# Optimization experiments

Measured on AMD Instinct MI355X. Metric: run time of the kernel, lower is better.

The kernel has to match this reference:

```python
import math
import jax, jax.numpy as jnp
import numpy as np

# ---- static config (mirrors init_kwargs) ----
NLAT_I, NLON_I = 240, 480      # input equiangular grid (incl. both poles)
NLAT_O, NLON_O = 361, 720      # output equiangular grid (incl. both poles)
CI, CO = 32, 32
NR, NPHI = 3, 3                # kernel_shape
K = (NR - 1) * NPHI + 1        # anisotropic piecewise-linear DISCO basis size = 7
LMAX = 120
CUTOFF = (NR + 0.25) * math.pi / LMAX     # _compute_cutoff_radius
DLAT_O = math.pi / (NLAT_O - 1)
WOFF = int(math.ceil(CUTOFF / DLAT_O))    # half lat-window (=10); geodesic dist >= |dtheta| so window is exact
WLAT = 2 * WOFF + 1
TWO_PI = 2.0 * math.pi


def _bilinear_upsample(x):
    # ResampleS2(mode='bilinear'): x [B,C,NLAT_I,NLON_I] -> [B,C,NLAT_O,NLON_O]
    # equiangular colatitudes theta_j = pi*j/(nlat-1); periodic longitude.
    pos_t = jnp.linspace(0.0, math.pi, NLAT_O) / (math.pi / (NLAT_I - 1))
    i0 = jnp.clip(jnp.floor(pos_t).astype(jnp.int32), 0, NLAT_I - 1)
    i1 = jnp.minimum(i0 + 1, NLAT_I - 1)
    wt = (pos_t - i0).astype(x.dtype)
    xl = (1.0 - wt)[:, None] * x[:, :, i0, :] + wt[:, None] * x[:, :, i1, :]
    pos_p = (jnp.arange(NLON_O) * (TWO_PI / NLON_O)) / (TWO_PI / NLON_I)
    j0f = jnp.floor(pos_p)
    j0 = j0f.astype(jnp.int32) % NLON_I
    j1 = (j0 + 1) % NLON_I
    wp = (pos_p - j0f).astype(x.dtype)
    return (1.0 - wp) * xl[..., j0] + wp * xl[..., j1]


def _build_psi():
    # DISCO filter tensor psi[k, t_out, dlat, dlon] with quadrature merged in,
    # exploiting longitude translation invariance (computed at lon_out = 0).
    theta = jnp.linspace(0.0, math.pi, NLAT_O)
    t_idx = jnp.arange(NLAT_O)
    d_idx = jnp.arange(WLAT) - WOFF
    lat_in = t_idx[:, None] + d_idx[None, :]             # [T,W]
    valid = (lat_in >= 0) & (lat_in < NLAT_O)
    lat_in_c = jnp.clip(lat_in, 0, NLAT_O - 1)
    alpha = -theta[:, None, None]                         # [T,1,1]
    gamma = theta[lat_in_c][:, :, None]                   # [T,W,1]
    beta = (TWO_PI / NLON_O) * jnp.arange(NLON_O)[None, None, :]
    # rotate input point into frame where the output point is at the north pole
    z = jnp.cos(alpha) * jnp.cos(gamma) - jnp.cos(beta) * jnp.sin(alpha) * jnp.sin(gamma)
    xx = jnp.cos(alpha) * jnp.cos(beta) * jnp.sin(gamma) + jnp.sin(alpha) * jnp.cos(gamma)
    yy = jnp.sin(beta) * jnp.sin(gamma)
    r = jnp.arccos(jnp.clip(z, -1.0, 1.0))                # geodesic distance [T,W,P]
    phi = jnp.arctan2(yy, xx) % TWO_PI                    # local azimuth
    dr = CUTOFF / NR
    dph = TWO_PI / NPHI
    vals = [jnp.maximum(0.0, 1.0 - r / dr)]               # isotropic center hat
    for k in range(1, K):
        ir = (k - 1) // NPHI + 1
        ip = (k - 1) % NPHI
        rad = jnp.maximum(0.0, 1.0 - jnp.abs(r - ir * dr) / dr)
        dd = jnp.abs(phi - ip * dph)
        dd = jnp.minimum(dd, TWO_PI - dd)
        az = jnp.maximum(0.0, 1.0 - dd / dph)
        vals.append(rad * az)
    psi = jnp.stack(vals, 0)                              # [K,T,W,P]
    psi = psi * (r <= CUTOFF) * valid[None, :, :, None]
    # merge quadrature weights of the input grid (sin(theta) dtheta dphi)
    q = jnp.sin(theta) * (math.pi / (NLAT_O - 1)) * (TWO_PI / NLON_O)
    psi = psi * q[lat_in_c][None, :, :, None]
    # nodal L1 normalization per basis function and output node
    scale = jnp.sum(psi, axis=(2, 3), keepdims=True)
    psi = psi / jnp.maximum(scale, 1e-8)
    return psi.astype(jnp.float32), lat_in_c


def _disco_conv(xu, weight, psi, lat_in_c):
    # xu [B,Ci,T,P]; weight [Co,Ci,K]; psi [K,T,W,P]
    h = jnp.einsum('oik,bitp->boktp', weight, xu)         # fold channel mixing first
    Hh = jnp.fft.rfft(h, axis=-1)                         # [B,Co,K,T,F]
    Ph = jnp.conj(jnp.fft.rfft(psi, axis=-1))             # [K,T,W,F]
    yh = jnp.zeros(Hh.shape[:2] + (NLAT_O, Hh.shape[-1]), dtype=Hh.dtype)
    for d in range(WLAT):                                 # small fixed halo loop
        Hd = Hh[:, :, :, lat_in_c[:, d], :]               # [B,Co,K,T,F]
        yh = yh + jnp.einsum('boktf,ktf->botf', Hd, Ph[:, :, d, :])
    return jnp.fft.irfft(yh, n=NLON_O, axis=-1)           # circular correlation over lon


def setup_inputs() -> dict:
    key = jax.random.key(0)
    k1, k2 = jax.random.split(key)
    x = jax.random.normal(k1, (1, CI, NLAT_I, NLON_I), dtype=jnp.float32)
    weight = jax.random.normal(k2, (CO, CI, K), dtype=jnp.float32) * 0.05
    return {'x': x, 'weight': weight}


def reference(x, weight):
    psi, lat_in_c = _build_psi()
    xu = _bilinear_upsample(x.astype(jnp.float32))        # forced fp32 region
    y = _disco_conv(xu, weight.astype(jnp.float32), psi, lat_in_c)
    return y.astype(x.dtype)
```

## Files before the change

kernel.cpp:

```cpp
#include <hip/hip_runtime.h>
#include <hip/hip_bf16.h>
#include <math.h>

#define NLAT_I 240
#define NLON_I 480
#define NLAT_O 361
#define NLON_O 720
#define CI_N 32
#define CO_N 32
#define K_N 7
#define WOFF 10
#define WLAT 21

#define PI_F 3.14159265358979323846f
#define TWOPI_F 6.28318530717958647692f
#define DLAT_V (PI_F / 360.0f)
#define DPHI_V (TWOPI_F / 720.0f)
#define CUTOFF_V (3.25f * PI_F / 120.0f)
#define DR_V (CUTOFF_V / 3.0f)
#define IDR_V (1.0f / DR_V)
#define DPH_V (TWOPI_F / 3.0f)
#define IDPH_V (1.0f / DPH_V)
#define QF_V (DLAT_V * DPHI_V)

#define PAD_T 64
#define CT 128
#define NBLK 256
#define NC45 45
#define NE 7581

typedef __attribute__((ext_vector_type(8))) short short8v;
typedef __attribute__((ext_vector_type(4))) short short4v;
typedef __attribute__((ext_vector_type(16))) float f32x16;

__device__ __forceinline__ unsigned short f2bf(float f) {
  __hip_bfloat16 h = __float2bfloat16(f);
  union { __hip_bfloat16 b; unsigned short s; } u; u.b = h; return u.s;
}

typedef __attribute__((address_space(1))) const unsigned int ga_u32_t;
typedef __attribute__((address_space(3))) unsigned int ls_u32_t;
__device__ __forceinline__ void dma16(const unsigned short* g, unsigned short* l) {
  __builtin_amdgcn_global_load_lds((ga_u32_t*)(const void*)g,
                                   (ls_u32_t*)(void*)l, 16, 0, 0);
}

__device__ __forceinline__ void psi_eval(float ct, float st, float cg, float sg,
                                         float q, float bang, float v[7]) {
  float sb, cb;
  sincosf(bang, &sb, &cb);
  float dx = sg * cb - st;
  float dy = sg * sb;
  float dz = cg - ct;
  float c2 = dx * dx + dy * dy + dz * dz;
  float r = 2.0f * asinf(fminf(1.0f, 0.5f * sqrtf(c2)));
  if (r <= CUTOFF_V) {
    float xx = ct * cb * sg - st * cg;
    float yy = sb * sg;
    float phi = atan2f(yy, xx);
    if (phi < 0.0f) phi += TWOPI_F;
    v[0] = fmaxf(0.0f, 1.0f - r * IDR_V) * q;
#pragma unroll
    for (int k = 1; k < 7; ++k) {
      const float irdr = (float)(1 + (k - 1) / 3) * DR_V;
      const float ipph = (float)((k - 1) % 3) * DPH_V;
      float rad = fmaxf(0.0f, 1.0f - fabsf(r - irdr) * IDR_V);
      float dd = fabsf(phi - ipph);
      dd = fminf(dd, TWOPI_F - dd);
      float az = fmaxf(0.0f, 1.0f - dd * IDPH_V);
      v[k] = rad * az * q;
    }
  } else {
#pragma unroll
    for (int k = 0; k < 7; ++k) v[k] = 0.0f;
  }
}

__device__ __forceinline__ int windowB(int t, int d) {
  int tp = t + d - WOFF;
  if (tp < 0 || tp > NLAT_O - 1) return -1;
  float th = (float)t * DLAT_V, ga = (float)tp * DLAT_V;
  float st = sinf(th), ct = cosf(th), sg = sinf(ga), cg = cosf(ga);
  float den = st * sg;
  float num = cosf(CUTOFF_V) - ct * cg;
  if (den < 1e-9f) return (fabsf(th - ga) <= CUTOFF_V) ? 360 : -1;
  if (num >= den) return -1;
  if (num <= -den) return 360;
  int B = (int)ceilf(acosf(num / den) * (1.0f / DPHI_V)) + 1;
  return B > 360 ? 360 : B;
}

__device__ __forceinline__ int nsupOf(int B) { return (B >= 360) ? 720 : 2 * B + 1; }
__device__ __forceinline__ int widthOf(int B) {
  return (B < 0) ? 0 : ((nsupOf(B) + 129) & ~1);
}

__global__ void prep_kernel(const float* __restrict__ w, unsigned short* __restrict__ w2,
                            int* __restrict__ offsF, int* __restrict__ offsT,
                            int* __restrict__ wtab, float* __restrict__ sums,
                            int* __restrict__ counter, int* __restrict__ gB,
                            int* __restrict__ gUc) {
  const int tid = threadIdx.x;
  __shared__ int temp[256];
  if (tid < 8) counter[tid] = 0;
  for (int idx = tid; idx < 361 * 7; idx += 256) sums[idx] = 0.0f;
  for (int idx = tid; idx < 14 * 32 * 16; idx += 256) {
    int kk = idx & 15; int o = (idx >> 4) & 31; int c16 = idx >> 9;
    int il = 4 * (kk >> 3) + (kk & 3) + 8 * ((kk >> 2) & 1);
    int i = (c16 & 1) * 16 + il; int k = c16 >> 1;
    w2[idx] = f2bf(w[(o * 32 + i) * 7 + k]);
  }
  for (int e = tid; e < NE; e += 256) {
    int t = e / 21, d = e % 21;
    int B = windowB(t, d);
    gB[e] = B;
    offsF[e] = (B >= 0) ? nsupOf(B) * 7 : 0;
    offsT[e] = 14 * widthOf(B);
  }
  __syncthreads();
  for (int t = tid; t < 361; t += 256) {
    int run = 0;
    for (int d = 0; d < WLAT; ++d) {
      gUc[t * 22 + d] = run;
      int B = gB[t * 21 + d];
      int np = (B >= 0) ? ((31 + B) >> 4) + ((B + 15) >> 4) + 1 : 0;
      run += np;
    }
    gUc[t * 22 + 21] = run;
    wtab[t] = run;
  }
  __syncthreads();
#pragma unroll 1
  for (int pass = 0; pass < 2; ++pass) {
    int* a = pass ? offsT : offsF;
    int s = tid * 30, e = s + 30; if (e > NE) e = NE; if (s > NE) s = NE;
    int sum = 0;
    for (int i = s; i < e; ++i) sum += a[i];
    temp[tid] = sum;
    __syncthreads();
    if (tid == 0) {
      int run = 0;
      for (int i = 0; i < 256; ++i) { int v = temp[i]; temp[i] = run; run += v; }
      a[NE] = run;
    }
    __syncthreads();
    int run = temp[tid];
    for (int i = s; i < e; ++i) { int v = a[i]; a[i] = run; run += v; }
    __syncthreads();
  }
}

__global__ void upsample_kernel(const float* __restrict__ x,
                                unsigned short* __restrict__ XT) {
  int idx = blockIdx.x * 256 + threadIdx.x;
  if (idx >= NLAT_O * NC45 * 512) return;
  int kk = idx & 15;
  int i = (idx >> 4) & 31;
  int c = (idx >> 9) % NC45;
  int t = idx / (NC45 * 512);
  int p = c * 16 + kk;

  double post = (double)t * (239.0 / 360.0);
  int i0 = (int)floor(post);
  if (i0 < 0) i0 = 0;
  if (i0 > NLAT_I - 1) i0 = NLAT_I - 1;
  int i1 = i0 + 1; if (i1 > NLAT_I - 1) i1 = NLAT_I - 1;
  float wt = (float)(post - (double)i0);

  double posp = (double)p * (2.0 / 3.0);
  double j0f = floor(posp);
  int j0 = ((int)j0f) % NLON_I;
  int j1 = (j0 + 1) % NLON_I;
  float wp = (float)(posp - j0f);

  const float* xi = x + (size_t)i * (NLAT_I * NLON_I);
  float a = xi[i0 * NLON_I + j0];
  float b = xi[i0 * NLON_I + j1];
  float cc = xi[i1 * NLON_I + j0];
  float d = xi[i1 * NLON_I + j1];
  float l0 = (1.0f - wt) * a + wt * cc;
  float l1 = (1.0f - wt) * b + wt * d;
  XT[idx] = f2bf((1.0f - wp) * l0 + wp * l1);
}

__global__ void psi_raw_kernel(const int* __restrict__ offsF,
                               float* __restrict__ PSIF,
                               float* __restrict__ sums) {
  int t = blockIdx.x, d = blockIdx.y;
  int B = windowB(t, d);
  if (B < 0) return;
  int nsup = nsupOf(B);
  int bLo = (B >= 360) ? -360 : -B;
  int offF = offsF[t * 21 + d];
  int tp = t + d - WOFF;
  float th = (float)t * DLAT_V, ga = (float)tp * DLAT_V;
  float st, ct, sg, cg;
  sincosf(th, &st, &ct);
  sincosf(ga, &sg, &cg);
  float q = sg * QF_V;
  float acc[7];
#pragma unroll
  for (int k = 0; k < 7; ++k) acc[k] = 0.0f;
  for (int ix = threadIdx.x; ix < nsup; ix += 256) {
    float v[7];
    psi_eval(ct, st, cg, sg, q, (float)(bLo + ix) * DPHI_V, v);
#pragma unroll
    for (int k = 0; k < 7; ++k) { PSIF[offF + k * nsup + ix] = v[k]; acc[k] += v[k]; }
  }
#pragma unroll
  for (int k = 0; k < 7; ++k) {
    float a = acc[k];
    for (int off = 32; off > 0; off >>= 1) a += __shfl_down(a, off, 64);
    acc[k] = a;
  }
  __shared__ float red[4][7];
  int wid = threadIdx.x >> 6;
  if ((threadIdx.x & 63) == 0) {
#pragma unroll
    for (int k = 0; k < 7; ++k) red[wid][k] = acc[k];
  }
  __syncthreads();
  if (threadIdx.x == 0) {
#pragma unroll
    for (int k = 0; k < 7; ++k)
      atomicAdd(&sums[t * 7 + k], red[0][k] + red[1][k] + red[2][k] + red[3][k]);
  }
}

__global__ void psi_toep_kernel(const int* __restrict__ offsF,
                                const int* __restrict__ offsT,
                                const float* __restrict__ PSIF,
                                const float* __restrict__ sums,
                                unsigned short* __restrict__ PSIT) {
  int t = blockIdx.x, d = blockIdx.y;
  int B = windowB(t, d);
  if (B < 0) return;
  int nsup = nsupOf(B);
  int width = widthOf(B);
  int offF = offsF[t * 21 + d];
  int offT = offsT[t * 21 + d];
  float rc[7];
#pragma unroll
  for (int k = 0; k < 7; ++k) rc[k] = 1.0f / fmaxf(sums[t * 7 + k], 1e-8f);
  for (int ix = threadIdx.x; ix <= width; ix += 256) {
    int isup = ix - PAD_T;
    unsigned short vv[7];
    if (isup >= 0 && isup < nsup) {
#pragma unroll
      for (int k = 0; k < 7; ++k)
        vv[k] = f2bf(PSIF[offF + k * nsup + isup] * rc[k]);
    } else {
#pragma unroll
      for (int k = 0; k < 7; ++k) vv[k] = 0;
    }
    if (ix < width) {
#pragma unroll
      for (int k = 0; k < 7; ++k) PSIT[offT + (2 * k) * width + ix] = vv[k];
    }
    if (ix >= 1) {
#pragma unroll
      for (int k = 0; k < 7; ++k) PSIT[offT + (2 * k + 1) * width + ix - 1] = vv[k];
    }
  }
}


#define VMW8 asm volatile("s_waitcnt vmcnt(8)" ::: "memory");
#define BARR  __builtin_amdgcn_s_barrier();

#define GETMETA(IX) \
    int mx_, my_; \
    if ((IX) & 64) { mx_ = __builtin_amdgcn_readlane(mxL1, (IX) & 63); \
                     my_ = __builtin_amdgcn_readlane(myL1, (IX) & 63); } \
    else           { mx_ = __builtin_amdgcn_readlane(mxL0, (IX) & 63); \
                     my_ = __builtin_amdgcn_readlane(myL0, (IX) & 63); }

#define STAGEU(IDX) {                                                       \
    int ix_ = (IDX); if (ix_ > nUm1) ix_ = nUm1;                            \
    GETMETA(ix_)                                                            \
    int wdt_ = my_ & 4095;                                                  \
    int dd_ = (my_ >> 12) & 31;                                             \
    int cc_ = ((my_ >> 17) & 63) - 32;                                      \
    int sl_ = ix_ & 7;                                                      \
    int jb_ = mx_ + lconst;                                                 \
    const unsigned short* bs_ = PSIT + jb_ + ((jb_ & 1) ? (wdt_ - 1) : 0);  \
    unsigned short* bd_ = Bring + sl_ * 3584;                               \
    int ks_ = 2 * wdt_;                                                     \
    dma16(bs_ + r0B * ks_, bd_ + (r0B << 9));                               \
    dma16(bs_ + r1B * ks_, bd_ + (r1B << 9));                               \
    int v45_ = pw16 + cc_;                                                  \
    if (v45_ < 0) v45_ += NC45;                                             \
    if (v45_ >= NC45) v45_ -= NC45;                                         \
    int v45b_ = v45_ + 2; if (v45b_ >= NC45) v45b_ -= NC45;                 \
    int tpd_ = t + dd_ - WOFF;                                              \
    unsigned short* ad_ = Aring + (((wv << 3) + sl_) << 10);                \
    dma16(XT + (((size_t)(tpd_ * NC45 + v45_)) << 9) + laneA, ad_);         \
    dma16(XT + (((size_t)(tpd_ * NC45 + v45b_)) << 9) + laneA, ad_ + 512); }

#define READF(S, IDX) {                                                     \
    int sl_ = (IDX) & 7;                                                    \
    const unsigned short* bb_ = Bring + sl_ * 3584 + (lane << 3);           \
    B##S##0 = *(const short8v*)(bb_);                                       \
    B##S##1 = *(const short8v*)(bb_ + 512);                                 \
    B##S##2 = *(const short8v*)(bb_ + 1024);                                \
    B##S##3 = *(const short8v*)(bb_ + 1536);                                \
    B##S##4 = *(const short8v*)(bb_ + 2048);                                \
    B##S##5 = *(const short8v*)(bb_ + 2560);                                \
    B##S##6 = *(const short8v*)(bb_ + 3072);                                \
    const unsigned short* aa_ = Aring + (((wv << 3) + sl_) << 10) + (lane << 3); \
    A##S##a = *(const short8v*)(aa_);                                       \
    A##S##b = *(const short8v*)(aa_ + 512); }

#define MFMA14(S) {                                                         \
    accA0 = __builtin_amdgcn_mfma_f32_32x32x16_bf16(A##S##a, B##S##0, accA0, 0, 0, 0); \
    accB0 = __builtin_amdgcn_mfma_f32_32x32x16_bf16(A##S##b, B##S##0, accB0, 0, 0, 0); \
    accA1 = __builtin_amdgcn_mfma_f32_32x32x16_bf16(A##S##a, B##S##1, accA1, 0, 0, 0); \
    accB1 = __builtin_amdgcn_mfma_f32_32x32x16_bf16(A##S##b, B##S##1, accB1, 0, 0, 0); \
    accA2 = __builtin_amdgcn_mfma_f32_32x32x16_bf16(A##S##a, B##S##2, accA2, 0, 0, 0); \
    accB2 = __builtin_amdgcn_mfma_f32_32x32x16_bf16(A##S##b, B##S##2, accB2, 0, 0, 0); \
    accA3 = __builtin_amdgcn_mfma_f32_32x32x16_bf16(A##S##a, B##S##3, accA3, 0, 0, 0); \
    accB3 = __builtin_amdgcn_mfma_f32_32x32x16_bf16(A##S##b, B##S##3, accB3, 0, 0, 0); \
    accA4 = __builtin_amdgcn_mfma_f32_32x32x16_bf16(A##S##a, B##S##4, accA4, 0, 0, 0); \
    accB4 = __builtin_amdgcn_mfma_f32_32x32x16_bf16(A##S##b, B##S##4, accB4, 0, 0, 0); \
    accA5 = __builtin_amdgcn_mfma_f32_32x32x16_bf16(A##S##a, B##S##5, accA5, 0, 0, 0); \
    accB5 = __builtin_amdgcn_mfma_f32_32x32x16_bf16(A##S##b, B##S##5, accB5, 0, 0, 0); \
    accA6 = __builtin_amdgcn_mfma_f32_32x32x16_bf16(A##S##a, B##S##6, accA6, 0, 0, 0); \
    accB6 = __builtin_amdgcn_mfma_f32_32x32x16_bf16(A##S##b, B##S##6, accB6, 0, 0, 0); }

#define DUMP2(ACC, KK, HB) {                                              \
    short8v q_;                                                           \
    q_[0]=(short)f2bf(ACC[8*(HB)+0]); q_[1]=(short)f2bf(ACC[8*(HB)+1]);   \
    q_[2]=(short)f2bf(ACC[8*(HB)+2]); q_[3]=(short)f2bf(ACC[8*(HB)+3]);   \
    q_[4]=(short)f2bf(ACC[8*(HB)+4]); q_[5]=(short)f2bf(ACC[8*(HB)+5]);   \
    q_[6]=(short)f2bf(ACC[8*(HB)+6]); q_[7]=(short)f2bf(ACC[8*(HB)+7]);   \
    *(short8v*)(b2 + ((KK) << 9) + b0_) = q_; }

#define GEMM2PT(AC0, AC1, AC2, AC3, AC4, AC5, AC6, PTILE) {               \
    f32x16 Dy;                                                            \
    _Pragma("unroll") for (int z = 0; z < 16; ++z) Dy[z] = 0.0f;          \
    DUMP2(AC0, 0, 0) DUMP2(AC1, 1, 0) DUMP2(AC2, 2, 0) DUMP2(AC3, 3, 0)  \
    DUMP2(AC4, 4, 0) DUMP2(AC5, 5, 0) DUMP2(AC6, 6, 0)                    \
    _Pragma("unroll") for (int k2 = 0; k2 < 7; ++k2) {                    \
      short8v A2 = *(const short8v*)(w2g + (((2 * k2 + 0) * 32 + nn) << 4) + g8); \
      short8v B2f = *(const short8v*)(b2 + (k2 << 9) + (nn << 4) + g8);   \
      Dy = __builtin_amdgcn_mfma_f32_32x32x16_bf16(A2, B2f, Dy, 0, 0, 0); \
    }                                                                     \
    DUMP2(AC0, 0, 1) DUMP2(AC1, 1, 1) DUMP2(AC2, 2, 1) DUMP2(AC3, 3, 1)  \
    DUMP2(AC4, 4, 1) DUMP2(AC5, 5, 1) DUMP2(AC6, 6, 1)                    \
    _Pragma("unroll") for (int k2 = 0; k2 < 7; ++k2) {                    \
      short8v A2 = *(const short8v*)(w2g + (((2 * k2 + 1) * 32 + nn) << 4) + g8); \
      short8v B2f = *(const short8v*)(b2 + (k2 << 9) + (nn << 4) + g8);   \
      Dy = __builtin_amdgcn_mfma_f32_32x32x16_bf16(A2, B2f, Dy, 0, 0, 0); \
    }                                                                     \
    const int p_ = (PTILE) * 32 + nn;                                     \
    if (p_ < NLON_O) {                                                    \
      _Pragma("unroll") for (int rr = 0; rr < 16; ++rr) {                 \
        int o = (rr & 3) + 8 * (rr >> 2) + 4 * g;                         \
        atomicAdd(&y[((size_t)o * NLAT_O + t) * NLON_O + p_], Dy[rr]);    \
      }                                                                   \
    } }

__global__ __launch_bounds__(256, 1) void disco_kernel(
    const unsigned short* __restrict__ XT, const unsigned short* __restrict__ PSIT,
    const unsigned short* __restrict__ w2g, const int* __restrict__ offsT,
    const int* __restrict__ wtab, const int* __restrict__ gB,
    const int* __restrict__ gUc, float* __restrict__ y,
    int* __restrict__ counter) {
  const int tid = threadIdx.x;
  __shared__ __align__(16) unsigned short Bring[8 * 3584];
  __shared__ __align__(16) unsigned short Aring[32 * 1024];
  __shared__ __align__(16) unsigned short b2all[4 * 3584];
  __shared__ int Sbuf[362];
  __shared__ int sB[WLAT], sUc[WLAT + 1], sOff[WLAT], sW[WLAT];
  __shared__ int curItem, sSv;

  for (int j = tid; j < 361; j += 256) {
    int t = (j & 1) ? 360 - (j >> 1) : (j >> 1);
    Sbuf[j] = 3 * ((wtab[t] + CT - 1) / CT);
  }
  __syncthreads();
  if (tid == 0) {
    int run = 0;
    for (int j = 0; j < 361; ++j) { int v = Sbuf[j]; Sbuf[j] = run; run += v; }
    Sbuf[361] = run;
    sSv = 0;
  }
  __syncthreads();
  const int NTOT = Sbuf[361];
  const int xcd = blockIdx.x & 7;

  const int lane = tid & 63, wv = tid >> 6, nn = lane & 31, g = lane >> 5;
  const int g8 = g * 8;
  const int laneA = nn * 16 + g8;
  const int lconst = g8 - nn;
  const int r0B = (wv < 3) ? 2 * wv : 6;
  const int r1B = (wv < 3) ? 2 * wv + 1 : 6;

  while (true) {
    if (tid == 0) {
      int mm = NTOT;
      int s2 = sSv;
      while (s2 < 8) {
        int cx = (xcd + s2) & 7;
        int b0 = (NTOT * cx) >> 3;
        int b1 = (NTOT * (cx + 1)) >> 3;
        int off = atomicAdd(&counter[cx], 1);
        if (b0 + off < b1) { mm = b0 + off; break; }
        ++s2;
      }
      sSv = s2;
      curItem = mm;
    }
    __syncthreads();
    const int m = curItem;
    if (m >= NTOT) break;

    int lo = 0, hi = 360;
    while (lo < hi) {
      int mid = (lo + hi + 1) >> 1;
      if (Sbuf[mid] <= m) lo = mid; else hi = mid - 1;
    }
    const int j = lo;
    const int r = m - Sbuf[j];
    const int t = (j & 1) ? 360 - (j >> 1) : (j >> 1);
    const int pgpair = r % 3;
    const int part = r / 3;

    if (tid < WLAT) {
      int B = gB[t * 21 + tid];
      sB[tid] = B;
      sOff[tid] = offsT[t * 21 + tid];
      sW[tid] = widthOf(B);
    }
    if (tid < WLAT + 1) sUc[tid] = gUc[t * 22 + tid];
    __syncthreads();

    const int Wt = sUc[WLAT];
    int g0 = part * CT, g1 = g0 + CT;
    if (g1 > Wt) g1 = Wt;
    const int nU = g1 - g0;
    const int nUm1 = nU - 1;

    const int ptileA = pgpair * 8 + 2 * wv;
    const int pw16 = ptileA * 2;

    int mxL0, myL0, mxL1, myL1;
#pragma unroll
    for (int hfu = 0; hfu < 2; ++hfu) {
      int uu_ = lane + hfu * 64; if (uu_ > nUm1) uu_ = nUm1;
      int ug_ = g0 + uu_;
      int dd = 0;
      while (dd < 20 && sUc[dd + 1] <= ug_) ++dd;
      int Bv = sB[dd];
      int bLo_ = (Bv >= 360) ? -360 : -Bv;
      int cc_ = -((Bv + 15) >> 4) + (ug_ - sUc[dd]);
      int mxv = sOff[dd] + cc_ * 16 - bLo_ + PAD_T;
      int myv = sW[dd] | (dd << 12) | ((cc_ + 32) << 17);
      if (hfu == 0) { mxL0 = mxv; myL0 = myv; } else { mxL1 = mxv; myL1 = myv; }
    }

    f32x16 accA0, accA1, accA2, accA3, accA4, accA5, accA6;
    f32x16 accB0, accB1, accB2, accB3, accB4, accB5, accB6;
#pragma unroll
    for (int z = 0; z < 16; ++z) {
      accA0[z]=0; accA1[z]=0; accA2[z]=0; accA3[z]=0; accA4[z]=0; accA5[z]=0; accA6[z]=0;
      accB0[z]=0; accB1[z]=0; accB2[z]=0; accB3[z]=0; accB4[z]=0; accB5[z]=0; accB6[z]=0;
    }

    short8v AXa, AXb, BX0, BX1, BX2, BX3, BX4, BX5, BX6;
    short8v AYa, AYb, BY0, BY1, BY2, BY3, BY4, BY5, BY6;

    STAGEU(0) STAGEU(1) STAGEU(2) STAGEU(3)
    VMW8 BARR
    READF(X, 0)

    int u = 0;
    while (true) {
      STAGEU(u + 4) STAGEU(u + 5)
      VMW8 BARR
      int nx = u + 1; bool h1 = (nx < nU); if (!h1) nx = u;
      READF(Y, nx)
      MFMA14(X)
      if (!h1) break;
      int nx2 = u + 2; bool h2 = (nx2 < nU); if (!h2) nx2 = nx;
      READF(X, nx2)
      MFMA14(Y)
      if (!h2) break;
      u += 2;
    }

    unsigned short* b2 = b2all + wv * 3584;
    const int b0_ = nn * 16 + g8;
    GEMM2PT(accA0, accA1, accA2, accA3, accA4, accA5, accA6, ptileA)
    GEMM2PT(accB0, accB1, accB2, accB3, accB4, accB5, accB6, ptileA + 1)
  }
}

extern "C" void kernel_launch(void* const* d_in, const int* in_sizes, int n_in,
                              void* d_out, int out_size, void* d_ws, size_t ws_size,
                              hipStream_t stream) {
  (void)in_sizes; (void)n_in; (void)out_size; (void)ws_size;
  const float* x = (const float*)d_in[0];
  const float* w = (const float*)d_in[1];
  float* y = (float*)d_out;

  unsigned short* XT = (unsigned short*)d_ws;
  float* PSIF = (float*)(XT + (size_t)NLAT_O * NC45 * 512);
  unsigned short* PSIT = (unsigned short*)(PSIF + 6000000);
  unsigned short* w2 = PSIT + 26000000;
  float* sums = (float*)(w2 + 7168);
  int* offsF = (int*)(sums + NLAT_O * K_N);
  int* offsT = offsF + NE + 1;
  int* wtab = offsT + NE + 1;
  int* counter = wtab + 361;
  int* gB = counter + 8;
  int* gUc = gB + NE;

  hipMemsetAsync(y, 0, (size_t)CO_N * NLAT_O * NLON_O * sizeof(float), stream);

  prep_kernel<<<1, 256, 0, stream>>>(w, w2, offsF, offsT, wtab, sums, counter, gB, gUc);
  int n_up = NLAT_O * NC45 * 512;
  upsample_kernel<<<(n_up + 255) / 256, 256, 0, stream>>>(x, XT);
  psi_raw_kernel<<<dim3(NLAT_O, WLAT), 256, 0, stream>>>(offsF, PSIF, sums);
  psi_toep_kernel<<<dim3(NLAT_O, WLAT), 256, 0, stream>>>(offsF, offsT, PSIF, sums, PSIT);
  disco_kernel<<<NBLK, 256, 0, stream>>>(XT, PSIT, w2, offsT, wtab, gB, gUc, y, counter);
}
```

Baseline: 478.0 us.

## Widen per-wave register tile to three longitude tiles, reusing psi fragments

Each wave now accumulates three 32-wide longitude tiles instead of two. Each psi B fragment read from LDS therefore feeds three MFMAs rather than two, and work items per latitude are regrouped from thirds into halves. To make room for the wider A ring, the separate epilogue scratch buffer is dropped and the second-stage GEMM now stages through the wave's own A-ring slots. This adds 112 accumulator registers and cuts the number of schedulable work items, which may hurt load balance. Async prefetches still in flight when the loop exits could also land on the reused scratch.

```diff
diff --git a/kernel.cpp b/kernel.cpp
--- a/kernel.cpp
+++ b/kernel.cpp
@@ -265,7 +265,7 @@
 }
 
 
-#define VMW8 asm volatile("s_waitcnt vmcnt(8)" ::: "memory");
+#define VMW10 asm volatile("s_waitcnt vmcnt(10)" ::: "memory");
 #define BARR  __builtin_amdgcn_s_barrier();
 
 #define GETMETA(IX) \
@@ -292,10 +292,13 @@
     if (v45_ < 0) v45_ += NC45;                                             \
     if (v45_ >= NC45) v45_ -= NC45;                                         \
     int v45b_ = v45_ + 2; if (v45b_ >= NC45) v45b_ -= NC45;                 \
+    int v45c_ = v45b_ + 2; if (v45c_ >= NC45) v45c_ -= NC45;                \
     int tpd_ = t + dd_ - WOFF;                                              \
-    unsigned short* ad_ = Aring + (((wv << 3) + sl_) << 10);                \
-    dma16(XT + (((size_t)(tpd_ * NC45 + v45_)) << 9) + laneA, ad_);         \
-    dma16(XT + (((size_t)(tpd_ * NC45 + v45b_)) << 9) + laneA, ad_ + 512); }
+    const unsigned short* ab_ = XT + (((size_t)(tpd_ * NC45)) << 9) + laneA; \
+    unsigned short* ad_ = Aring + (((wv << 3) + sl_) * 1536);               \
+    dma16(ab_ + ((size_t)v45_ << 9), ad_);                                  \
+    dma16(ab_ + ((size_t)v45b_ << 9), ad_ + 512);                           \
+    dma16(ab_ + ((size_t)v45c_ << 9), ad_ + 1024); }
 
 #define READF(S, IDX) {                                                     \
     int sl_ = (IDX) & 7;                                                    \
@@ -307,25 +310,33 @@
     B##S##4 = *(const short8v*)(bb_ + 2048);                                \
     B##S##5 = *(const short8v*)(bb_ + 2560);                                \
     B##S##6 = *(const short8v*)(bb_ + 3072);                                \
-    const unsigned short* aa_ = Aring + (((wv << 3) + sl_) << 10) + (lane << 3); \
+    const unsigned short* aa_ = Aring + (((wv << 3) + sl_) * 1536) + (lane << 3); \
     A##S##a = *(const short8v*)(aa_);                                       \
-    A##S##b = *(const short8v*)(aa_ + 512); }
-
-#define MFMA14(S) {                                                         \
+    A##S##b = *(const short8v*)(aa_ + 512);                                 \
+    A##S##c = *(const short8v*)(aa_ + 1024); }
+
+#define MFMA21(S) {                                                         \
     accA0 = __builtin_amdgcn_mfma_f32_32x32x16_bf16(A##S##a, B##S##0, accA0, 0, 0, 0); \
     accB0 = __builtin_amdgcn_mfma_f32_32x32x16_bf16(A##S##b, B##S##0, accB0, 0, 0, 0); \
+    accC0 = __builtin_amdgcn_mfma_f32_32x32x16_bf16(A##S##c, B##S##0, accC0, 0, 0, 0); \
     accA1 = __builtin_amdgcn_mfma_f32_32x32x16_bf16(A##S##a, B##S##1, accA1, 0, 0, 0); \
     accB1 = __builtin_amdgcn_mfma_f32_32x32x16_bf16(A##S##b, B##S##1, accB1, 0, 0, 0); \
+    accC1 = __builtin_amdgcn_mfma_f32_32x32x16_bf16(A##S##c, B##S##1, accC1, 0, 0, 0); \
     accA2 = __builtin_amdgcn_mfma_f32_32x32x16_bf16(A##S##a, B##S##2, accA2, 0, 0, 0); \
     accB2 = __builtin_amdgcn_mfma_f32_32x32x16_bf16(A##S##b, B##S##2, accB2, 0, 0, 0); \
+    accC2 = __builtin_amdgcn_mfma_f32_32x32x16_bf16(A##S##c, B##S##2, accC2, 0, 0, 0); \
     accA3 = __builtin_amdgcn_mfma_f32_32x32x16_bf16(A##S##a, B##S##3, accA3, 0, 0, 0); \
     accB3 = __builtin_amdgcn_mfma_f32_32x32x16_bf16(A##S##b, B##S##3, accB3, 0, 0, 0); \
+    accC3 = __builtin_amdgcn_mfma_f32_32x32x16_bf16(A##S##c, B##S##3, accC3, 0, 0, 0); \
     accA4 = __builtin_amdgcn_mfma_f32_32x32x16_bf16(A##S##a, B##S##4, accA4, 0, 0, 0); \
     accB4 = __builtin_amdgcn_mfma_f32_32x32x16_bf16(A##S##b, B##S##4, accB4, 0, 0, 0); \
+    accC4 = __builtin_amdgcn_mfma_f32_32x32x16_bf16(A##S##c, B##S##4, accC4, 0, 0, 0); \
     accA5 = __builtin_amdgcn_mfma_f32_32x32x16_bf16(A##S##a, B##S##5, accA5, 0, 0, 0); \
     accB5 = __builtin_amdgcn_mfma_f32_32x32x16_bf16(A##S##b, B##S##5, accB5, 0, 0, 0); \
+    accC5 = __builtin_amdgcn_mfma_f32_32x32x16_bf16(A##S##c, B##S##5, accC5, 0, 0, 0); \
     accA6 = __builtin_amdgcn_mfma_f32_32x32x16_bf16(A##S##a, B##S##6, accA6, 0, 0, 0); \
-    accB6 = __builtin_amdgcn_mfma_f32_32x32x16_bf16(A##S##b, B##S##6, accB6, 0, 0, 0); }
+    accB6 = __builtin_amdgcn_mfma_f32_32x32x16_bf16(A##S##b, B##S##6, accB6, 0, 0, 0); \
+    accC6 = __builtin_amdgcn_mfma_f32_32x32x16_bf16(A##S##c, B##S##6, accC6, 0, 0, 0); }
 
 #define DUMP2(ACC, KK, HB) {                                              \
     short8v q_;                                                           \
@@ -368,15 +379,14 @@
     int* __restrict__ counter) {
   const int tid = threadIdx.x;
   __shared__ __align__(16) unsigned short Bring[8 * 3584];
-  __shared__ __align__(16) unsigned short Aring[32 * 1024];
-  __shared__ __align__(16) unsigned short b2all[4 * 3584];
+  __shared__ __align__(16) unsigned short Aring[8 * 4 * 1536];
   __shared__ int Sbuf[362];
   __shared__ int sB[WLAT], sUc[WLAT + 1], sOff[WLAT], sW[WLAT];
   __shared__ int curItem, sSv;
 
   for (int j = tid; j < 361; j += 256) {
     int t = (j & 1) ? 360 - (j >> 1) : (j >> 1);
-    Sbuf[j] = 3 * ((wtab[t] + CT - 1) / CT);
+    Sbuf[j] = 2 * ((wtab[t] + CT - 1) / CT);
   }
   __syncthreads();
   if (tid == 0) {
@@ -423,8 +433,8 @@
     const int j = lo;
     const int r = m - Sbuf[j];
     const int t = (j & 1) ? 360 - (j >> 1) : (j >> 1);
-    const int pgpair = r % 3;
-    const int part = r / 3;
+    const int pghalf = r & 1;
+    const int part = r >> 1;
 
     if (tid < WLAT) {
       int B = gB[t * 21 + tid];
@@ -441,7 +451,7 @@
     const int nU = g1 - g0;
     const int nUm1 = nU - 1;
 
-    const int ptileA = pgpair * 8 + 2 * wv;
+    const int ptileA = pghalf * 12 + wv * 3;
     const int pw16 = ptileA * 2;
 
     int mxL0, myL0, mxL1, myL1;
@@ -461,38 +471,41 @@
 
     f32x16 accA0, accA1, accA2, accA3, accA4, accA5, accA6;
     f32x16 accB0, accB1, accB2, accB3, accB4, accB5, accB6;
+    f32x16 accC0, accC1, accC2, accC3, accC4, accC5, accC6;
 #pragma unroll
     for (int z = 0; z < 16; ++z) {
       accA0[z]=0; accA1[z]=0; accA2[z]=0; accA3[z]=0; accA4[z]=0; accA5[z]=0; accA6[z]=0;
       accB0[z]=0; accB1[z]=0; accB2[z]=0; accB3[z]=0; accB4[z]=0; accB5[z]=0; accB6[z]=0;
-    }
-
-    short8v AXa, AXb, BX0, BX1, BX2, BX3, BX4, BX5, BX6;
-    short8v AYa, AYb, BY0, BY1, BY2, BY3, BY4, BY5, BY6;
+      accC0[z]=0; accC1[z]=0; accC2[z]=0; accC3[z]=0; accC4[z]=0; accC5[z]=0; accC6[z]=0;
+    }
+
+    short8v AXa, AXb, AXc, BX0, BX1, BX2, BX3, BX4, BX5, BX6;
+    short8v AYa, AYb, AYc, BY0, BY1, BY2, BY3, BY4, BY5, BY6;
 
     STAGEU(0) STAGEU(1) STAGEU(2) STAGEU(3)
-    VMW8 BARR
+    VMW10 BARR
     READF(X, 0)
 
     int u = 0;
     while (true) {
       STAGEU(u + 4) STAGEU(u + 5)
-      VMW8 BARR
+      VMW10 BARR
       int nx = u + 1; bool h1 = (nx < nU); if (!h1) nx = u;
       READF(Y, nx)
-      MFMA14(X)
+      MFMA21(X)
       if (!h1) break;
       int nx2 = u + 2; bool h2 = (nx2 < nU); if (!h2) nx2 = nx;
       READF(X, nx2)
-      MFMA14(Y)
+      MFMA21(Y)
       if (!h2) break;
       u += 2;
     }
 
-    unsigned short* b2 = b2all + wv * 3584;
+    unsigned short* b2 = Aring + wv * (8 * 1536);
     const int b0_ = nn * 16 + g8;
     GEMM2PT(accA0, accA1, accA2, accA3, accA4, accA5, accA6, ptileA)
     GEMM2PT(accB0, accB1, accB2, accB3, accB4, accB5, accB6, ptileA + 1)
+    GEMM2PT(accC0, accC1, accC2, accC3, accC4, accC5, accC6, ptileA + 2)
   }
 }
 
```

Result: slower. 929.6 us (+94.5%).
